# Kernel optimization log

Measured on AMD Instinct MI355X. Metric: run time of the kernel, lower is better.

The kernel has to match this reference:

```python
import jax, jax.numpy as jnp
import numpy as np

B, M, IN, H = 4096, 16, 512, 512


def _linear_params(key, out_dim, in_dim):
    kw, kb = jax.random.split(key)
    s = 1.0 / np.sqrt(in_dim)
    W = jax.random.uniform(kw, (out_dim, in_dim), jnp.float32, -s, s)
    b = jax.random.uniform(kb, (out_dim,), jnp.float32, -s, s)
    return W, b


def setup_inputs() -> dict:
    key = jax.random.key(0)
    ks = jax.random.split(key, 15)
    inp = {
        "input": jax.random.normal(ks[0], (B, IN), jnp.float32),
        "h0": jax.random.normal(ks[1], (B, H), jnp.float32),
        "c0": jax.random.normal(ks[2], (B, H), jnp.float32),
        "all_c_b_e_w": jax.random.normal(ks[3], (B, M, H), jnp.float32),
        "all_num_word": jax.random.randint(ks[4], (B,), 0, M + 1, jnp.int32),
    }
    names = ["ii", "hi", "if_", "hf", "ig", "hg", "io", "ho", "lx", "lc"]
    in_dims = [IN, H, IN, H, IN, H, IN, H, IN, H]
    for n, d, k in zip(names, in_dims, ks[5:15]):
        W, b = _linear_params(k, H, d)
        inp["W_" + n] = W
        inp["b_" + n] = b
    return inp


def _lin(x, W, b):
    return x @ W.T + b


def reference(input, h0, c0, all_c_b_e_w, all_num_word,
              W_ii, b_ii, W_hi, b_hi, W_if_, b_if_, W_hf, b_hf,
              W_ig, b_ig, W_hg, b_hg, W_io, b_io, W_ho, b_ho,
              W_lx, b_lx, W_lc, b_lc):
    i = jax.nn.sigmoid(_lin(input, W_ii, b_ii) + _lin(h0, W_hi, b_hi))   # [B,H]
    f = jax.nn.sigmoid(_lin(input, W_if_, b_if_) + _lin(h0, W_hf, b_hf))  # computed but unused, as in original
    g = jnp.tanh(_lin(input, W_ig, b_ig) + _lin(h0, W_hg, b_hg))         # [B,H]
    o = jax.nn.sigmoid(_lin(input, W_io, b_io) + _lin(h0, W_ho, b_ho))   # [B,H]

    # lattice word-cell gates, vectorized over the ragged word dim with a mask
    lx = _lin(input, W_lx, b_lx)                 # [B,H]
    lc = _lin(all_c_b_e_w, W_lc, b_lc)           # [B,M,H]
    i_b = jax.nn.sigmoid(lx[:, None, :] + lc)    # [B,M,H]
    mask = (jnp.arange(M)[None, :] < all_num_word[:, None])  # [B,M]
    exp_b = jnp.exp(i_b) * mask[:, :, None].astype(i_b.dtype)  # [B,M,H]
    exp_i = jnp.exp(i)                                         # [B,H]
    denom = exp_i + jnp.sum(exp_b, axis=1)                     # [B,H]
    c_words = jnp.sum((exp_b / denom[:, None, :]) * all_c_b_e_w, axis=1)
    c_lat = c_words + (exp_i / denom) * g
    c = jnp.where((all_num_word > 0)[:, None], c_lat, g)       # num_word==0 -> c=g
    h1 = o * jnp.tanh(c)
    return (h1, c)
```

## Files before the change

kernel.cpp:

```cpp
#include <hip/hip_runtime.h>
#include <hip/hip_bf16.h>
#include <stdint.h>


typedef __attribute__((ext_vector_type(8))) short short8;
typedef __attribute__((ext_vector_type(4))) float f32x4;
typedef __attribute__((ext_vector_type(4))) unsigned short us4;

__device__ __forceinline__ unsigned short f2bf(float f) {
  union { float f; unsigned u; } v; v.f = f;
  return (unsigned short)((v.u + 0x7fffu + ((v.u >> 16) & 1u)) >> 16);
}
__device__ __forceinline__ unsigned short f2bf_h(float f) {
  __hip_bfloat16 h = __float2bfloat16(f);
  return *reinterpret_cast<unsigned short*>(&h);
}
__device__ __forceinline__ float bf2f(unsigned short u) {
  return __uint_as_float((unsigned)u << 16);
}
__device__ __forceinline__ float sigmoidf_(float x) {
  return 1.f / (1.f + __expf(-x));
}
__device__ __forceinline__ float fast_tanh(float x) {
  float e = __expf(-2.f * fmaxf(x, -30.f));
  return (1.f - e) / (1.f + e);
}

__global__ void k_cvt_all(const float* __restrict__ x, const float* __restrict__ h,
                          const float* __restrict__ Wii, const float* __restrict__ Wig,
                          const float* __restrict__ Wio, const float* __restrict__ Wlx,
                          const float* __restrict__ Whi, const float* __restrict__ Whg,
                          const float* __restrict__ Who, const float* __restrict__ Wlcf,
                          unsigned short* __restrict__ XH, unsigned short* __restrict__ Wcat,
                          unsigned short* __restrict__ Wlc) {
  const int bb = blockIdx.x;
  const int tid = threadIdx.x;
  us4 o;
  if (bb < 4096) {
    const int t = bb * 256 + tid;
    const int b = t >> 8;
    const int col = (t & 255) * 4;
    const float* src = (col < 512) ? (x + (size_t)b * 512 + col)
                                   : (h + (size_t)b * 512 + (col - 512));
    f32x4 v = *(const f32x4*)src;
    o[0] = f2bf(v[0]); o[1] = f2bf(v[1]); o[2] = f2bf(v[2]); o[3] = f2bf(v[3]);
    *(us4*)(XH + (size_t)t * 4) = o;
  } else if (bb < 6144) {
    const int t = (bb - 4096) * 256 + tid;
    const int row = t >> 8;
    const int col = (t & 255) * 4;
    const int sec = row >> 9, r = row & 511;
    if (col < 512) {
      const float* W = sec == 0 ? Wii : sec == 1 ? Wig : sec == 2 ? Wio : Wlx;
      f32x4 v = *(const f32x4*)(W + (size_t)r * 512 + col);
      o[0] = f2bf(v[0]); o[1] = f2bf(v[1]); o[2] = f2bf(v[2]); o[3] = f2bf(v[3]);
    } else if (sec < 3) {
      const float* W = sec == 0 ? Whi : sec == 1 ? Whg : Who;
      f32x4 v = *(const f32x4*)(W + (size_t)r * 512 + (col - 512));
      o[0] = f2bf(v[0]); o[1] = f2bf(v[1]); o[2] = f2bf(v[2]); o[3] = f2bf(v[3]);
    } else {
      o[0] = 0; o[1] = 0; o[2] = 0; o[3] = 0;
    }
    *(us4*)(Wcat + (size_t)t * 4) = o;
  } else {
    const int t = (bb - 6144) * 256 + tid;
    f32x4 v = *(const f32x4*)(Wlcf + (size_t)t * 4);
    o[0] = f2bf(v[0]); o[1] = f2bf(v[1]); o[2] = f2bf(v[2]); o[3] = f2bf(v[3]);
    *(us4*)(Wlc + (size_t)t * 4) = o;
  }
}

__global__ __launch_bounds__(256) void k_gemm0(
    const unsigned short* __restrict__ A, const unsigned short* __restrict__ Bm,
    unsigned short* __restrict__ C, int Ndim, int Kdim, int nbx) {
  __shared__ unsigned short As[2][128 * 64];
  __shared__ unsigned short Bs[2][128 * 64];
  const int tid = threadIdx.x;
  const int lane = tid & 63, wid = tid >> 6;
  const int wr = wid >> 1, wc = wid & 1;
  const int l15 = lane & 15, lhi = lane >> 4;

  const int chunk = gridDim.x >> 3;
  const int bid = (blockIdx.x & 7) * chunk + (blockIdx.x >> 3);
  const int brow = bid / nbx, bcol = bid % nbx;
  const int m0 = brow * 128, n0 = bcol * 128;

  f32x4 acc[4][4];
#pragma unroll
  for (int i = 0; i < 4; ++i)
#pragma unroll
    for (int j = 0; j < 4; ++j) acc[i][j] = (f32x4){0.f, 0.f, 0.f, 0.f};

  const int cb0 = wid * 64;
  auto stage = [&](int buf, int k0) {
#pragma unroll
    for (int q = 0; q < 4; ++q) {
      const int cb = q * 256 + cb0;
      const int chunkid = cb + lane;
      const int row = chunkid >> 3, slot = chunkid & 7;
      const int kk = k0 + ((slot ^ (row & 7)) << 3);
      __builtin_amdgcn_global_load_lds(
          (const __attribute__((address_space(1))) unsigned int*)(A + (size_t)(m0 + row) * Kdim + kk),
          (__attribute__((address_space(3))) unsigned int*)(As[buf] + cb * 8), 16, 0, 0);
      __builtin_amdgcn_global_load_lds(
          (const __attribute__((address_space(1))) unsigned int*)(Bm + (size_t)(n0 + row) * Kdim + kk),
          (__attribute__((address_space(3))) unsigned int*)(Bs[buf] + cb * 8), 16, 0, 0);
    }
  };

  const int nt = Kdim >> 6;
  stage(0, 0);
  __syncthreads();

  const int swz = (lane & 7) << 4;
  for (int t = 0; t < nt; ++t) {
    const int cur = t & 1;
    if (t + 1 < nt) stage(cur ^ 1, (t + 1) << 6);
    const char* Ab = (const char*)As[cur];
    const char* Bb = (const char*)Bs[cur];
#pragma unroll
    for (int s = 0; s < 2; ++s) {
      short8 av[4], bv[4];
#pragma unroll
      for (int mi = 0; mi < 4; ++mi) {
        const int row = wr * 64 + mi * 16 + l15;
        av[mi] = *(const short8*)(Ab + row * 128 + ((s * 64 + lhi * 16) ^ swz));
      }
#pragma unroll
      for (int ni = 0; ni < 4; ++ni) {
        const int row = wc * 64 + ni * 16 + l15;
        bv[ni] = *(const short8*)(Bb + row * 128 + ((s * 64 + lhi * 16) ^ swz));
      }
#pragma unroll
      for (int mi = 0; mi < 4; ++mi)
#pragma unroll
        for (int ni = 0; ni < 4; ++ni)
          acc[mi][ni] = __builtin_amdgcn_mfma_f32_16x16x32_bf16(av[mi], bv[ni], acc[mi][ni], 0, 0, 0);
    }
    __syncthreads();
  }

#pragma unroll
  for (int mi = 0; mi < 4; ++mi) {
    const int gr = m0 + wr * 64 + mi * 16 + lhi * 4;
#pragma unroll
    for (int ni = 0; ni < 4; ++ni) {
      const int gc = n0 + wc * 64 + ni * 16 + l15;
#pragma unroll
      for (int j = 0; j < 4; ++j)
        C[(size_t)(gr + j) * Ndim + gc] = f2bf(acc[mi][ni][j]);
    }
  }
}

__global__ __launch_bounds__(512) void k_latg(
    const float* __restrict__ Af,
    const unsigned short* __restrict__ Bm,
    const int* __restrict__ num_word,
    unsigned short* __restrict__ lcb) {
  __shared__ unsigned short As[2][256 * 32];
  __shared__ unsigned short Bs[2][256 * 32];
  const int tid = threadIdx.x;
  const int lane = tid & 63, wid = tid >> 6;
  const int wrow = wid >> 2, wcol = wid & 3;
  const int l15 = lane & 15, lhi = lane >> 4;

  const int chunk = gridDim.x >> 3;
  const int bid = (blockIdx.x & 7) * chunk + (blockIdx.x >> 3);
  const int brow = bid >> 1, bcol = bid & 1;
  const int m0 = brow * 256, n0 = bcol * 256;

  f32x4 acc[8][4];
#pragma unroll
  for (int i = 0; i < 8; ++i)
#pragma unroll
    for (int j = 0; j < 4; ++j) acc[i][j] = (f32x4){0.f, 0.f, 0.f, 0.f};

  f32x4 SA[2][2], SB[2][2];

  auto loadA = [&](f32x4 (&dst)[2][2], int k0) {
#pragma unroll
    for (int q = 0; q < 2; ++q) {
      const int c = q * 512 + tid;
      const int row = c >> 2, s = c & 3;
      const float* p = Af + (size_t)(m0 + row) * 512 + k0 + s * 8;
      dst[q][0] = *(const f32x4*)p;
      dst[q][1] = *(const f32x4*)(p + 4);
    }
  };
  auto writeA = [&](int buf, f32x4 (&src)[2][2]) {
#pragma unroll
    for (int q = 0; q < 2; ++q) {
      const int c = q * 512 + tid;
      const int row = c >> 2, s = c & 3;
      const int pr = row >> 1;
      const int phys = (s + ((row & 1) << 2)) ^ (pr & 7);
      short8 v;
      v[0] = (short)f2bf_h(src[q][0][0]); v[1] = (short)f2bf_h(src[q][0][1]);
      v[2] = (short)f2bf_h(src[q][0][2]); v[3] = (short)f2bf_h(src[q][0][3]);
      v[4] = (short)f2bf_h(src[q][1][0]); v[5] = (short)f2bf_h(src[q][1][1]);
      v[6] = (short)f2bf_h(src[q][1][2]); v[7] = (short)f2bf_h(src[q][1][3]);
      *(short8*)((char*)As[buf] + pr * 128 + phys * 16) = v;
    }
  };
  auto stageB = [&](int buf, int k0) {
#pragma unroll
    for (int q = 0; q < 2; ++q) {
      const int cb = q * 512 + wid * 64;
      const int c = cb + lane;
      const int pr = c >> 3, phys = c & 7;
      const int gi = phys ^ (pr & 7);
      const int row = pr * 2 + (gi >> 2);
      const int kk = k0 + ((gi & 3) << 3);
      __builtin_amdgcn_global_load_lds(
          (const __attribute__((address_space(1))) unsigned int*)(Bm + (size_t)(n0 + row) * 512 + kk),
          (__attribute__((address_space(3))) unsigned int*)(Bs[buf] + cb * 8), 16, 0, 0);
    }
  };

  auto compute = [&](int buf) {
    const char* Ab = (const char*)As[buf];
    const char* Bb = (const char*)Bs[buf];
    short8 av[8], bv[4];
#pragma unroll
    for (int mi = 0; mi < 8; ++mi) {
      const int row = wrow * 128 + mi * 16 + l15;
      const int pr = row >> 1;
      av[mi] = *(const short8*)(Ab + pr * 128 +
                (((lhi + ((row & 1) << 2)) ^ (pr & 7)) << 4));
    }
#pragma unroll
    for (int ni = 0; ni < 4; ++ni) {
      const int row = wcol * 64 + ni * 16 + l15;
      const int pr = row >> 1;
      bv[ni] = *(const short8*)(Bb + pr * 128 +
                (((lhi + ((row & 1) << 2)) ^ (pr & 7)) << 4));
    }
#pragma unroll
    for (int mi = 0; mi < 8; ++mi)
#pragma unroll
      for (int ni = 0; ni < 4; ++ni)
        acc[mi][ni] = __builtin_amdgcn_mfma_f32_16x16x32_bf16(av[mi], bv[ni], acc[mi][ni], 0, 0, 0);
  };

  loadA(SA, 0);
  loadA(SB, 32);
  stageB(0, 0);
  writeA(0, SA);
  __syncthreads();

#pragma unroll
  for (int t = 0; t < 16; t += 2) {
    if (t + 2 < 16) loadA(SA, (t + 2) << 5);
    if (t + 1 < 16) stageB(1, (t + 1) << 5);
    compute(0);
    if (t + 1 < 16) writeA(1, SB);
    __syncthreads();
    if (t + 3 < 16) loadA(SB, (t + 3) << 5);
    if (t + 2 < 16) stageB(0, (t + 2) << 5);
    compute(1);
    if (t + 2 < 16) writeA(0, SA);
    __syncthreads();
  }

#pragma unroll
  for (int mi = 0; mi < 8; ++mi) {
    const int rbase = m0 + wrow * 128 + mi * 16;
    const int nw = num_word[rbase >> 4];
    const int gr = rbase + lhi * 4;
#pragma unroll
    for (int ni = 0; ni < 4; ++ni) {
      const int gc = n0 + wcol * 64 + ni * 16 + l15;
#pragma unroll
      for (int j = 0; j < 4; ++j)
        if (lhi * 4 + j < nw)
          lcb[(size_t)(gr + j) * 512 + gc] = f2bf(acc[mi][ni][j]);
    }
  }
}

__global__ __launch_bounds__(512) void k_epi(
    const unsigned short* __restrict__ lc,
    const float* __restrict__ all_c,
    const unsigned short* __restrict__ C1u,
    const int* __restrict__ num_word,
    const float* __restrict__ b_ii, const float* __restrict__ b_hi,
    const float* __restrict__ b_ig, const float* __restrict__ b_hg,
    const float* __restrict__ b_io, const float* __restrict__ b_ho,
    const float* __restrict__ b_lx, const float* __restrict__ b_lc,
    float* __restrict__ outH, float* __restrict__ outC) {
  const int b = blockIdx.x;
  const int hc = threadIdx.x;
  const int nw = num_word[b];
  const size_t base = (size_t)b * 2048;

  const float pre = bf2f(C1u[base + 1536 + hc]) + b_lx[hc] + b_lc[hc];
  const unsigned short* lcp = lc + ((size_t)b * 16) * 512 + hc;
  const float* wp = all_c + ((size_t)b * 16) * 512 + hc;

  float se = 0.f, sew = 0.f;
#pragma unroll 4
  for (int m = 0; m < nw; ++m) {
    const float ib = sigmoidf_(pre + bf2f(lcp[(size_t)m * 512]));
    const float e = __expf(ib);
    se += e;
    sew += e * wp[(size_t)m * 512];
  }

  const float ig = sigmoidf_(bf2f(C1u[base + hc]) + b_ii[hc] + b_hi[hc]);
  const float g  = fast_tanh(bf2f(C1u[base + 512 + hc]) + b_ig[hc] + b_hg[hc]);
  const float og = sigmoidf_(bf2f(C1u[base + 1024 + hc]) + b_io[hc] + b_ho[hc]);
  const float ei = __expf(ig);
  const float denom = ei + se;
  const float cc = (sew + ei * g) / denom;
  outH[(size_t)b * 512 + hc] = og * fast_tanh(cc);
  outC[(size_t)b * 512 + hc] = cc;
}

extern "C" void kernel_launch(void* const* d_in, const int* in_sizes, int n_in,
                              void* d_out, int out_size, void* d_ws, size_t ws_size,
                              hipStream_t stream) {
  const float* input    = (const float*)d_in[0];
  const float* h0       = (const float*)d_in[1];
  const float* all_c    = (const float*)d_in[3];
  const int*   num_word = (const int*)d_in[4];
  const float* W_ii = (const float*)d_in[5];  const float* b_ii = (const float*)d_in[6];
  const float* W_hi = (const float*)d_in[7];  const float* b_hi = (const float*)d_in[8];
  const float* W_ig = (const float*)d_in[13]; const float* b_ig = (const float*)d_in[14];
  const float* W_hg = (const float*)d_in[15]; const float* b_hg = (const float*)d_in[16];
  const float* W_io = (const float*)d_in[17]; const float* b_io = (const float*)d_in[18];
  const float* W_ho = (const float*)d_in[19]; const float* b_ho = (const float*)d_in[20];
  const float* W_lx = (const float*)d_in[21]; const float* b_lx = (const float*)d_in[22];
  const float* W_lc = (const float*)d_in[23]; const float* b_lc = (const float*)d_in[24];

  char* ws = (char*)d_ws;
  unsigned short* XH   = (unsigned short*)(ws);
  unsigned short* Wcat = (unsigned short*)(ws + 8388608);
  unsigned short* Wlc  = (unsigned short*)(ws + 12582912);
  unsigned short* C1u  = (unsigned short*)(ws + 13107200);
  unsigned short* lc   = (unsigned short*)(ws + 29884416);

  float* outH = (float*)d_out;
  float* outC = outH + (size_t)4096 * 512;

  k_cvt_all<<<6400, 256, 0, stream>>>(input, h0, W_ii, W_ig, W_io, W_lx,
                                      W_hi, W_hg, W_ho, W_lc, XH, Wcat, Wlc);

  k_gemm0<<<512, 256, 0, stream>>>(XH, Wcat, C1u, 2048, 1024, 16);

  k_latg<<<512, 512, 0, stream>>>(all_c, Wlc, num_word, lc);

  k_epi<<<4096, 512, 0, stream>>>(lc, all_c, C1u, num_word,
      b_ii, b_hi, b_ig, b_hg, b_io, b_ho, b_lx, b_lc, outH, outC);
}
```

Before: 114.2 us.

## Stage fp32 A tile directly into LDS and convert to bf16 at compute

The A operand of the lattice GEMM is now copied straight from global memory into LDS as fp32 using async global_load_lds, with an XOR swizzle. This replaces the old path of loading into registers, converting to bf16 and writing LDS. Conversion to bf16 moves into the compute step, and the loop becomes a simple double-buffered, non-unrolled loop. The aim is to cut register staging and VALU work in the load path. In exchange, LDS use for A doubles, each of the four column waves converts the same A data again, and the larger LDS footprint may lower occupancy.

```diff
diff --git a/kernel.cpp b/kernel.cpp
--- a/kernel.cpp
+++ b/kernel.cpp
@@ -158,7 +158,7 @@
     const unsigned short* __restrict__ Bm,
     const int* __restrict__ num_word,
     unsigned short* __restrict__ lcb) {
-  __shared__ unsigned short As[2][256 * 32];
+  __shared__ float As[2][256 * 32];
   __shared__ unsigned short Bs[2][256 * 32];
   const int tid = threadIdx.x;
   const int lane = tid & 63, wid = tid >> 6;
@@ -176,31 +176,17 @@
 #pragma unroll
     for (int j = 0; j < 4; ++j) acc[i][j] = (f32x4){0.f, 0.f, 0.f, 0.f};
 
-  f32x4 SA[2][2], SB[2][2];
-
-  auto loadA = [&](f32x4 (&dst)[2][2], int k0) {
-#pragma unroll
-    for (int q = 0; q < 2; ++q) {
-      const int c = q * 512 + tid;
-      const int row = c >> 2, s = c & 3;
-      const float* p = Af + (size_t)(m0 + row) * 512 + k0 + s * 8;
-      dst[q][0] = *(const f32x4*)p;
-      dst[q][1] = *(const f32x4*)(p + 4);
-    }
-  };
-  auto writeA = [&](int buf, f32x4 (&src)[2][2]) {
-#pragma unroll
-    for (int q = 0; q < 2; ++q) {
-      const int c = q * 512 + tid;
-      const int row = c >> 2, s = c & 3;
-      const int pr = row >> 1;
-      const int phys = (s + ((row & 1) << 2)) ^ (pr & 7);
-      short8 v;
-      v[0] = (short)f2bf_h(src[q][0][0]); v[1] = (short)f2bf_h(src[q][0][1]);
-      v[2] = (short)f2bf_h(src[q][0][2]); v[3] = (short)f2bf_h(src[q][0][3]);
-      v[4] = (short)f2bf_h(src[q][1][0]); v[5] = (short)f2bf_h(src[q][1][1]);
-      v[6] = (short)f2bf_h(src[q][1][2]); v[7] = (short)f2bf_h(src[q][1][3]);
-      *(short8*)((char*)As[buf] + pr * 128 + phys * 16) = v;
+  auto stageA = [&](int buf, int k0) {
+#pragma unroll
+    for (int q = 0; q < 4; ++q) {
+      const int cb = q * 512 + wid * 64;
+      const int c = cb + lane;
+      const int row = c >> 3, phys = c & 7;
+      const int gi = phys ^ (row & 7);
+      const int kk = k0 + gi * 4;
+      __builtin_amdgcn_global_load_lds(
+          (const __attribute__((address_space(1))) unsigned int*)(Af + (size_t)(m0 + row) * 512 + kk),
+          (__attribute__((address_space(3))) unsigned int*)(As[buf] + cb * 4), 16, 0, 0);
     }
   };
   auto stageB = [&](int buf, int k0) {
@@ -221,13 +207,19 @@
   auto compute = [&](int buf) {
     const char* Ab = (const char*)As[buf];
     const char* Bb = (const char*)Bs[buf];
-    short8 av[8], bv[4];
+    short8 av[8];
+    short8 bv[4];
 #pragma unroll
     for (int mi = 0; mi < 8; ++mi) {
       const int row = wrow * 128 + mi * 16 + l15;
-      const int pr = row >> 1;
-      av[mi] = *(const short8*)(Ab + pr * 128 +
-                (((lhi + ((row & 1) << 2)) ^ (pr & 7)) << 4));
+      const int s0 = (2 * lhi) ^ (row & 7);
+      const int s1 = (2 * lhi + 1) ^ (row & 7);
+      const f32x4 a0 = *(const f32x4*)(Ab + row * 128 + s0 * 16);
+      const f32x4 a1 = *(const f32x4*)(Ab + row * 128 + s1 * 16);
+      av[mi][0] = (short)f2bf_h(a0[0]); av[mi][1] = (short)f2bf_h(a0[1]);
+      av[mi][2] = (short)f2bf_h(a0[2]); av[mi][3] = (short)f2bf_h(a0[3]);
+      av[mi][4] = (short)f2bf_h(a1[0]); av[mi][5] = (short)f2bf_h(a1[1]);
+      av[mi][6] = (short)f2bf_h(a1[2]); av[mi][7] = (short)f2bf_h(a1[3]);
     }
 #pragma unroll
     for (int ni = 0; ni < 4; ++ni) {
@@ -243,23 +235,18 @@
         acc[mi][ni] = __builtin_amdgcn_mfma_f32_16x16x32_bf16(av[mi], bv[ni], acc[mi][ni], 0, 0, 0);
   };
 
-  loadA(SA, 0);
-  loadA(SB, 32);
+  stageA(0, 0);
   stageB(0, 0);
-  writeA(0, SA);
   __syncthreads();
 
-#pragma unroll
-  for (int t = 0; t < 16; t += 2) {
-    if (t + 2 < 16) loadA(SA, (t + 2) << 5);
-    if (t + 1 < 16) stageB(1, (t + 1) << 5);
-    compute(0);
-    if (t + 1 < 16) writeA(1, SB);
-    __syncthreads();
-    if (t + 3 < 16) loadA(SB, (t + 3) << 5);
-    if (t + 2 < 16) stageB(0, (t + 2) << 5);
-    compute(1);
-    if (t + 2 < 16) writeA(0, SA);
+#pragma unroll 1
+  for (int t = 0; t < 16; ++t) {
+    const int cur = t & 1;
+    if (t + 1 < 16) {
+      stageA(cur ^ 1, (t + 1) << 5);
+      stageB(cur ^ 1, (t + 1) << 5);
+    }
+    compute(cur);
     __syncthreads();
   }
 
```

Result: slower. 122.4 us (+7.1%).
